# Kernel optimization log

Measured on AMD Instinct MI355X. Metric: run time of the kernel, lower is better.

## Reference

```python
import jax, jax.numpy as jnp
import numpy as np

B, S, F, D = 64, 129, 768, 4
MOM = 0.9
EPS = 1e-6


def setup_inputs() -> dict:
    key = jax.random.key(0)
    ks = jax.random.split(key, 8)
    x = jax.random.normal(ks[0], (B, S, F), dtype=jnp.float32)
    labels = jax.random.randint(ks[1], (B,), 0, 16, dtype=jnp.int32)
    domain = jax.random.randint(ks[2], (B,), 0, D, dtype=jnp.int32)
    lmda = jax.random.beta(ks[3], 0.1, 0.1, (B, 1, 1)).astype(jnp.float32)
    d_rand = jax.random.randint(ks[4], (B,), 1, D, dtype=jnp.int32)  # range(1, num_domains)
    mean_buf = (0.1 * jax.random.normal(ks[5], (D, F))).astype(jnp.float32)
    var_buf = jax.random.uniform(ks[6], (D, F), minval=0.5, maxval=1.5, dtype=jnp.float32)
    hg_noise = jax.random.normal(ks[7], (B, S, F), dtype=jnp.float32)
    return {"input": x, "lmda": lmda, "mean_buf": mean_buf, "var_buf": var_buf,
            "hg_noise": hg_noise, "labels": labels, "domain": domain, "d_rand": d_rand}


def reference(input, lmda, mean_buf, var_buf, hg_noise, labels, domain, d_rand):
    x = input  # [B,S,F]
    b, s, f = x.shape
    d = mean_buf.shape[0]

    # --- per-domain mean/var over dims [0,1] (unbiased), momentum buffer update ---
    tok = x.reshape(b * s, f)
    seg = jnp.repeat(domain, s)  # [B*S]
    cnt = jax.ops.segment_sum(jnp.ones((b * s,), x.dtype), seg, num_segments=d)  # tokens/domain
    s1 = jax.ops.segment_sum(tok, seg, num_segments=d)          # [D,F]
    s2 = jax.ops.segment_sum(tok * tok, seg, num_segments=d)    # [D,F]
    n = cnt[:, None]
    mu_d = s1 / jnp.maximum(n, 1.0)
    var_d = (s2 - n * mu_d * mu_d) / jnp.maximum(n - 1.0, 1.0)  # unbiased, matches torch.var
    present = (cnt > 0)[:, None]
    new_mean = jnp.where(present, MOM * mean_buf + (1.0 - MOM) * mu_d, mean_buf)
    new_var = jnp.where(present, MOM * var_buf + (1.0 - MOM) * var_d, var_buf)

    # --- instance renorm over token dim (unbiased var) + cross-domain restyle ---
    mu_i = x.mean(1, keepdims=True)
    v_i = x.var(1, keepdims=True, ddof=1)
    x_normed = (x - mu_i) * jax.lax.rsqrt(v_i + EPS)
    ds = (domain + d_rand) % d
    x_new = x_normed * jnp.sqrt(new_var[ds] + EPS)[:, None, :] + new_mean[ds][:, None, :]
    x_mix = lmda * x + (1.0 - lmda) * x_new

    # --- Gaussian hallucinated samples from own-domain stats ---
    hg = new_mean[domain][:, None, :] + jnp.sqrt(new_var[domain] + EPS)[:, None, :] * hg_noise

    # --- pairwise euclidean distance + hard example mining + soft-margin triplet loss ---
    xe = jnp.concatenate([x, x_mix, hg], axis=0).reshape(3 * b, s * f)  # [3B, S*F]
    ln = jnp.concatenate([labels, labels, -jnp.ones((b,), labels.dtype)])
    sq = jnp.sum(xe * xe, axis=1)
    d2 = sq[:, None] + sq[None, :] - 2.0 * (xe @ xe.T)
    dist = jnp.sqrt(jnp.clip(d2, 1e-12))
    pos = ln[:, None] == ln[None, :]
    big = jnp.asarray(1e30, dist.dtype)
    dist_ap = jnp.max(jnp.where(pos, dist, -big), axis=1)
    dist_an = jnp.min(jnp.where(pos, big, dist), axis=1)
    tri_hard_loss = jnp.mean(jax.nn.softplus(dist_ap - dist_an))  # SoftMarginLoss, y=1

    return x_mix, tri_hard_loss, new_mean, new_var
```

## Files before the change

### kernel.cpp

```cpp
#include <hip/hip_runtime.h>
#include <math.h>

#define B_ 64
#define S_ 129
#define F_ 768
#define N3 192
#define GSZ 36864
#define GRID_MAIN 252

#define WS_S1   0
#define WS_S2   49152
#define WS_PART 98304

#define OUT_LOSS 6340608
#define OUT_NM   6340609
#define OUT_NV   6343681

typedef unsigned int uint;
using short8v = __attribute__((ext_vector_type(8))) short;
using float4v = __attribute__((ext_vector_type(4))) float;

__global__ void k_stats(const float* __restrict__ x,
                        float* __restrict__ s1, float* __restrict__ s2,
                        float* __restrict__ out_loss) {
    __shared__ float4 r1[256], r2[256];
    if (blockIdx.x == 0 && threadIdx.x == 0) out_loss[0] = 0.0f;
    int b = blockIdx.x / 3, fg = blockIdx.x % 3;
    int c = threadIdx.x & 63, sp = threadIdx.x >> 6;
    int f = fg * 256 + c * 4;
    const float* p = x + (size_t)b * S_ * F_ + f;
    int s0 = sp * 32;
    int se = s0 + 32 + (sp == 3 ? 1 : 0);
    float4 a1 = {0.f,0.f,0.f,0.f}, a2 = {0.f,0.f,0.f,0.f};
#pragma unroll 4
    for (int s = s0; s < se; ++s) {
        float4 v = *(const float4*)(p + s * F_);
        a1.x += v.x; a1.y += v.y; a1.z += v.z; a1.w += v.w;
        a2.x += v.x*v.x; a2.y += v.y*v.y; a2.z += v.z*v.z; a2.w += v.w*v.w;
    }
    r1[threadIdx.x] = a1; r2[threadIdx.x] = a2;
    __syncthreads();
    if (sp == 0) {
        float4 t1 = r1[c], t2 = r2[c];
#pragma unroll
        for (int k = 1; k < 4; ++k) {
            float4 u1 = r1[k * 64 + c], u2 = r2[k * 64 + c];
            t1.x += u1.x; t1.y += u1.y; t1.z += u1.z; t1.w += u1.w;
            t2.x += u2.x; t2.y += u2.y; t2.z += u2.z; t2.w += u2.w;
        }
        *(float4*)(s1 + b * F_ + f) = t1;
        *(float4*)(s2 + b * F_ + f) = t2;
    }
}

__device__ __forceinline__ uint pack2(float a, float b) {
    uint ua = __float_as_uint(a);
    uint ub = __float_as_uint(b);
    uint ha = (ua + 0x7FFFu + ((ua >> 16) & 1u)) >> 16;
    uint hb = (ub + 0x7FFFu + ((ub >> 16) & 1u)) & 0xFFFF0000u;
    return hb | ha;
}

__device__ __forceinline__ void bf16_store8(char* lds, int row, int g,
                                            float4 v0, float4 v1) {
    uint4 H;
    H.x = pack2(v0.x, v0.y);
    H.y = pack2(v0.z, v0.w);
    H.z = pack2(v1.x, v1.y);
    H.w = pack2(v1.z, v1.w);
    *(uint4*)(lds + row * 128 + ((g ^ (row & 7)) << 4)) = H;
}

__device__ __forceinline__ float4 fma4(float4 a, float4 x, float4 b) {
    float4 r;
    r.x = fmaf(a.x, x.x, b.x); r.y = fmaf(a.y, x.y, b.y);
    r.z = fmaf(a.z, x.z, b.z); r.w = fmaf(a.w, x.w, b.w);
    return r;
}

template <bool EXCL>
__global__ __launch_bounds__(512, 2)
void k_main(const float* __restrict__ x, const float* __restrict__ hgn,
            const float* __restrict__ s1, const float* __restrict__ s2,
            const float* __restrict__ mean_buf, const float* __restrict__ var_buf,
            const float* __restrict__ lmda, const int* __restrict__ domain,
            const int* __restrict__ d_rand,
            float* __restrict__ xmix, float* __restrict__ out_nm,
            float* __restrict__ out_nv,
            float* part, int npart) {
    __shared__ __align__(16) char LDS[25088];
    __shared__ float NMV[4][64];
    __shared__ float SVV[4][64];

    int tid = threadIdx.x;
    int bid = blockIdx.x;
    int fc = bid % 12, sb = bid / 12;
    int f0 = fc * 64;
    int b = tid >> 3, g = tid & 7;
    int w = tid >> 6;
    int wr = (w >> 2) * 96, wc = (w & 3) * 48;
    int lane = tid & 63, m = lane & 15, qd = lane >> 4;

    int s = sb;
    size_t goff = ((size_t)b * S_ + s) * F_ + f0 + (g << 3);
    float4 X0 = ((const float4*)(x + goff))[0];
    float4 X1 = ((const float4*)(x + goff))[1];
    float4 N0 = ((const float4*)(hgn + goff))[0];
    float4 N1 = ((const float4*)(hgn + goff))[1];

    if (tid < 256) {
        int d = tid & 3, fl = tid >> 2;
        int f = f0 + fl;
        float a1 = 0.f, a2 = 0.f, cnt = 0.f;
#pragma unroll 8
        for (int bb = 0; bb < B_; ++bb) {
            bool mk = (domain[bb] == d);
            a1  += mk ? s1[bb * F_ + f] : 0.f;
            a2  += mk ? s2[bb * F_ + f] : 0.f;
            cnt += mk ? 1.f : 0.f;
        }
        float nm, nv;
        if (cnt > 0.f) {
            float n = cnt * (float)S_;
            float mu = a1 / n;
            float var = (a2 - n * mu * mu) / fmaxf(n - 1.f, 1.f);
            nm = 0.9f * mean_buf[d * F_ + f] + 0.1f * mu;
            nv = 0.9f * var_buf[d * F_ + f] + 0.1f * var;
        } else {
            nm = mean_buf[d * F_ + f];
            nv = var_buf[d * F_ + f];
        }
        NMV[d][fl] = nm;
        SVV[d][fl] = sqrtf(nv + 1e-6f);
        if (sb == 0) { out_nm[d * F_ + f] = nm; out_nv[d * F_ + f] = nv; }
    }
    __syncthreads();

    int cb = b * F_ + f0 + (g << 3);
    float4 S1a = ((const float4*)(s1 + cb))[0], S1b = ((const float4*)(s1 + cb))[1];
    float4 S2a = ((const float4*)(s2 + cb))[0], S2b = ((const float4*)(s2 + cb))[1];
    int dm = domain[b];
    int dsd = (dm + d_rand[b]) & 3;
    float lam = lmda[b];
    float4 C1a, C1b, C0a, C0b, HMa, HMb, HSa, HSb;
#define COEF(SC1, SC2, FL, RC1, RC0, RHM, RHS) {            \
        float mu = (SC1) * (1.0f / (float)S_);              \
        float v  = ((SC2) - (float)S_ * mu * mu) * (1.0f / (float)(S_ - 1)); \
        float r  = rsqrtf(v + 1e-6f);                       \
        float sv = SVV[dsd][FL];                            \
        float rs = r * sv;                                  \
        RC1 = lam + (1.0f - lam) * rs;                      \
        RC0 = (1.0f - lam) * (NMV[dsd][FL] - mu * rs);      \
        RHM = NMV[dm][FL];                                  \
        RHS = SVV[dm][FL]; }
    {
        int fb = g << 3;
        COEF(S1a.x, S2a.x, fb + 0, C1a.x, C0a.x, HMa.x, HSa.x);
        COEF(S1a.y, S2a.y, fb + 1, C1a.y, C0a.y, HMa.y, HSa.y);
        COEF(S1a.z, S2a.z, fb + 2, C1a.z, C0a.z, HMa.z, HSa.z);
        COEF(S1a.w, S2a.w, fb + 3, C1a.w, C0a.w, HMa.w, HSa.w);
        COEF(S1b.x, S2b.x, fb + 4, C1b.x, C0b.x, HMb.x, HSb.x);
        COEF(S1b.y, S2b.y, fb + 5, C1b.y, C0b.y, HMb.y, HSb.y);
        COEF(S1b.z, S2b.z, fb + 6, C1b.z, C0b.z, HMb.z, HSb.z);
        COEF(S1b.w, S2b.w, fb + 7, C1b.w, C0b.w, HMb.w, HSb.w);
    }
#undef COEF

    float4v acc[6][3];
#pragma unroll
    for (int i = 0; i < 6; ++i)
#pragma unroll
        for (int j = 0; j < 3; ++j)
            acc[i][j] = (float4v){0.f, 0.f, 0.f, 0.f};

    for (; s < S_; s += 21) {
        float4 M0 = fma4(C1a, X0, C0a);
        float4 M1 = fma4(C1b, X1, C0b);
        ((float4*)(xmix + goff))[0] = M0;
        ((float4*)(xmix + goff))[1] = M1;
        float4 H0 = fma4(HSa, N0, HMa);
        float4 H1 = fma4(HSb, N1, HMb);

        bf16_store8(LDS, b, g, X0, X1);
        bf16_store8(LDS, 64 + b, g, M0, M1);
        bf16_store8(LDS, 128 + b, g, H0, H1);
        __syncthreads();

        int sn = s + 21;
        if (sn < S_) {
            goff = ((size_t)b * S_ + sn) * F_ + f0 + (g << 3);
            X0 = ((const float4*)(x + goff))[0];
            X1 = ((const float4*)(x + goff))[1];
            N0 = ((const float4*)(hgn + goff))[0];
            N1 = ((const float4*)(hgn + goff))[1];
        }

#pragma unroll
        for (int t = 0; t < 2; ++t) {
            short8v A[6];
#pragma unroll
            for (int i = 0; i < 6; ++i) {
                int row = wr + i * 16 + m;
                int go = (((t << 2) + qd) ^ (row & 7)) << 4;
                A[i] = *(const short8v*)(LDS + row * 128 + go);
            }
#pragma unroll
            for (int j = 0; j < 3; ++j) {
                int row = wc + j * 16 + m;
                int go = (((t << 2) + qd) ^ (row & 7)) << 4;
                short8v Bv = *(const short8v*)(LDS + row * 128 + go);
#pragma unroll
                for (int i = 0; i < 6; ++i)
                    acc[i][j] = __builtin_amdgcn_mfma_f32_16x16x32_bf16(A[i], Bv, acc[i][j], 0, 0, 0);
            }
        }
        __syncthreads();
    }

    float* T = (float*)LDS;
    const int PADW = 196;
    float* dst = part + (size_t)(bid % npart) * GSZ;
    int lrb = (wr ? 16 : 0) + (qd << 2);
    int lr2 = tid >> 4;
#pragma unroll
    for (int i = 0; i < 6; ++i) {
        __syncthreads();
#pragma unroll
        for (int j = 0; j < 3; ++j) {
            int colb = wc + j * 16 + m;
#pragma unroll
            for (int r = 0; r < 4; ++r)
                T[(lrb + r) * PADW + colb] = acc[i][j][r];
        }
        __syncthreads();
        int grow = i * 16 + (lr2 & 15) + (lr2 >> 4) * 96;
#pragma unroll
        for (int k = 0; k < 3; ++k) {
            int c4 = k * 16 + (tid & 15);
            float4 vv = *(const float4*)&T[lr2 * PADW + (c4 << 2)];
            int o = grow * N3 + (c4 << 2);
            if (EXCL) {
                *(float4*)(dst + o) = vv;
            } else {
                atomicAdd(dst + o + 0, vv.x);
                atomicAdd(dst + o + 1, vv.y);
                atomicAdd(dst + o + 2, vv.z);
                atomicAdd(dst + o + 3, vv.w);
            }
        }
    }
}

__global__ void k_red(const float* __restrict__ part, float* __restrict__ gram, int npart) {
    int j = blockIdx.x * 256 + threadIdx.x;
    float s = 0.0f;
#pragma unroll 8
    for (int p = 0; p < npart; ++p) s += part[(size_t)p * GSZ + j];
    gram[j] = s;
}

__global__ void k_loss(const float* __restrict__ gram, const int* __restrict__ labels,
                       float* __restrict__ out_loss) {
    __shared__ float sq[N3];
    __shared__ int ln[N3];
    int i = blockIdx.x, lane = threadIdx.x;
    for (int k = lane; k < N3; k += 64) {
        sq[k] = gram[k * (N3 + 1)];
        ln[k] = (k < 128) ? labels[k & 63] : -1;
    }
    __syncthreads();
    int li = ln[i];
    float si = sq[i];
    float ap = -1e30f, an = 1e30f;
    for (int j = lane; j < N3; j += 64) {
        float d2 = si + sq[j] - 2.0f * gram[i * N3 + j];
        float dist = sqrtf(fmaxf(d2, 1e-12f));
        bool pos = (li == ln[j]);
        ap = pos ? fmaxf(ap, dist) : ap;
        an = pos ? an : fminf(an, dist);
    }
#pragma unroll
    for (int off = 32; off; off >>= 1) {
        ap = fmaxf(ap, __shfl_xor(ap, off));
        an = fminf(an, __shfl_xor(an, off));
    }
    if (lane == 0) {
        float xv = ap - an;
        float sp = fmaxf(xv, 0.0f) + log1pf(expf(-fabsf(xv)));
        atomicAdd(out_loss, sp * (1.0f / (float)N3));
    }
}

extern "C" void kernel_launch(void* const* d_in, const int* in_sizes, int n_in,
                              void* d_out, int out_size, void* d_ws, size_t ws_size,
                              hipStream_t stream) {
    const float* x        = (const float*)d_in[0];
    const float* lmda     = (const float*)d_in[1];
    const float* mean_buf = (const float*)d_in[2];
    const float* var_buf  = (const float*)d_in[3];
    const float* hgn      = (const float*)d_in[4];
    const int*   labels   = (const int*)d_in[5];
    const int*   domain   = (const int*)d_in[6];
    const int*   d_rand   = (const int*)d_in[7];
    float* out = (float*)d_out;
    float* ws  = (float*)d_ws;

    long avail = (long)(ws_size / 4) - WS_PART;
    int npart = (int)(avail / GSZ) - 1;
    if (npart < 1) npart = 1;
    if (npart > GRID_MAIN) npart = GRID_MAIN;
    bool excl = (npart == GRID_MAIN);
    float* part = ws + WS_PART;
    float* gram = ws + WS_PART + (size_t)npart * GSZ;

    k_stats<<<dim3(192), dim3(256), 0, stream>>>(x, ws + WS_S1, ws + WS_S2,
                                                 out + OUT_LOSS);
    if (!excl) {
        hipMemsetAsync(part, 0, (size_t)npart * GSZ * 4, stream);
    }
    if (excl) {
        k_main<true><<<dim3(GRID_MAIN), dim3(512), 0, stream>>>(
            x, hgn, ws + WS_S1, ws + WS_S2, mean_buf, var_buf,
            lmda, domain, d_rand,
            out, out + OUT_NM, out + OUT_NV, part, npart);
    } else {
        k_main<false><<<dim3(GRID_MAIN), dim3(512), 0, stream>>>(
            x, hgn, ws + WS_S1, ws + WS_S2, mean_buf, var_buf,
            lmda, domain, d_rand,
            out, out + OUT_NM, out + OUT_NV, part, npart);
    }
    k_red<<<dim3(144), dim3(256), 0, stream>>>(part, gram, npart);
    k_loss<<<dim3(N3), dim3(64), 0, stream>>>(gram, labels, out + OUT_LOSS);
}
```

Before: 154.2 us.

## Fuse stats, gram, reduction and loss into one cooperative kernel with grid syncs

Replaces the multi-kernel pipeline (stats kernel, main gram kernel, separate reduction and loss kernels) with a single cooperative launch that uses grid.sync between phases. The stats phase now spreads each block's token loop over 512 threads, and the partial-gram reduction plus triplet loss run inside the same kernel. The aim is to remove kernel launch gaps and inter-kernel idle time. The cost is grid-wide barriers, and it depends on cooperative launch succeeding with all 252 blocks resident, with the old path kept as a fallback.

Result: slower. 262.9 us (+70.5%).

```diff
diff --git a/kernel.cpp b/kernel.cpp
--- a/kernel.cpp
+++ b/kernel.cpp
@@ -1,5 +1,8 @@
 #include <hip/hip_runtime.h>
+#include <hip/hip_cooperative_groups.h>
 #include <math.h>
+
+namespace cg = cooperative_groups;
 
 #define B_ 64
 #define S_ 129
@@ -10,7 +13,8 @@
 
 #define WS_S1   0
 #define WS_S2   49152
-#define WS_PART 98304
+#define WS_SQ   98304
+#define WS_PART 98560
 
 #define OUT_LOSS 6340608
 #define OUT_NM   6340609
@@ -19,6 +23,285 @@
 typedef unsigned int uint;
 using short8v = __attribute__((ext_vector_type(8))) short;
 using float4v = __attribute__((ext_vector_type(4))) float;
+
+__device__ __forceinline__ uint pack2(float a, float b) {
+    uint ua = __float_as_uint(a);
+    uint ub = __float_as_uint(b);
+    uint ha = (ua + 0x7FFFu + ((ua >> 16) & 1u)) >> 16;
+    uint hb = (ub + 0x7FFFu + ((ub >> 16) & 1u)) & 0xFFFF0000u;
+    return hb | ha;
+}
+
+__device__ __forceinline__ void bf16_store8(char* lds, int row, int g,
+                                            float4 v0, float4 v1) {
+    uint4 H;
+    H.x = pack2(v0.x, v0.y);
+    H.y = pack2(v0.z, v0.w);
+    H.z = pack2(v1.x, v1.y);
+    H.w = pack2(v1.z, v1.w);
+    *(uint4*)(lds + row * 128 + ((g ^ (row & 7)) << 4)) = H;
+}
+
+__device__ __forceinline__ float4 fma4(float4 a, float4 x, float4 b) {
+    float4 r;
+    r.x = fmaf(a.x, x.x, b.x); r.y = fmaf(a.y, x.y, b.y);
+    r.z = fmaf(a.z, x.z, b.z); r.w = fmaf(a.w, x.w, b.w);
+    return r;
+}
+
+__global__ __launch_bounds__(512, 2)
+void k_all(const float* __restrict__ x, const float* __restrict__ hgn,
+           const float* __restrict__ mean_buf, const float* __restrict__ var_buf,
+           const float* __restrict__ lmda, const int* __restrict__ domain,
+           const int* __restrict__ d_rand, const int* __restrict__ labels,
+           float* __restrict__ xmix, float* __restrict__ out_nm,
+           float* __restrict__ out_nv, float* __restrict__ out_loss,
+           float* __restrict__ s1, float* __restrict__ s2,
+           float* __restrict__ sqw, float* part) {
+    __shared__ __align__(16) char LDS[32768];
+    __shared__ float NMV[4][64];
+    __shared__ float SVV[4][64];
+
+    cg::grid_group grid = cg::this_grid();
+    int tid = threadIdx.x;
+    int bid = blockIdx.x;
+
+    if (bid < 192) {
+        float4* r1 = (float4*)LDS;
+        float4* r2 = (float4*)(LDS + 8192);
+        int bb = bid / 3, fg = bid % 3;
+        int c = tid & 63, sp = tid >> 6;
+        int f = fg * 256 + c * 4;
+        const float* p = x + (size_t)bb * S_ * F_ + f;
+        int s0 = sp * 16;
+        int se = s0 + 16 + (sp == 7 ? 1 : 0);
+        float4 a1 = {0.f,0.f,0.f,0.f}, a2 = {0.f,0.f,0.f,0.f};
+#pragma unroll 4
+        for (int s = s0; s < se; ++s) {
+            float4 v = *(const float4*)(p + s * F_);
+            a1.x += v.x; a1.y += v.y; a1.z += v.z; a1.w += v.w;
+            a2.x += v.x*v.x; a2.y += v.y*v.y; a2.z += v.z*v.z; a2.w += v.w*v.w;
+        }
+        r1[tid] = a1; r2[tid] = a2;
+        __syncthreads();
+        if (sp == 0) {
+            float4 t1 = r1[c], t2 = r2[c];
+#pragma unroll
+            for (int k = 1; k < 8; ++k) {
+                float4 u1 = r1[k * 64 + c], u2 = r2[k * 64 + c];
+                t1.x += u1.x; t1.y += u1.y; t1.z += u1.z; t1.w += u1.w;
+                t2.x += u2.x; t2.y += u2.y; t2.z += u2.z; t2.w += u2.w;
+            }
+            *(float4*)(s1 + bb * F_ + f) = t1;
+            *(float4*)(s2 + bb * F_ + f) = t2;
+        }
+    }
+    grid.sync();
+
+    {
+        int fc = bid % 12, sb = bid / 12;
+        int f0 = fc * 64;
+        int b = tid >> 3, g = tid & 7;
+        int w = tid >> 6;
+        int wr = (w >> 2) * 96, wc = (w & 3) * 48;
+        int lane = tid & 63, m = lane & 15, qd = lane >> 4;
+
+        int s = sb;
+        size_t goff = ((size_t)b * S_ + s) * F_ + f0 + (g << 3);
+        float4 X0 = ((const float4*)(x + goff))[0];
+        float4 X1 = ((const float4*)(x + goff))[1];
+        float4 N0 = ((const float4*)(hgn + goff))[0];
+        float4 N1 = ((const float4*)(hgn + goff))[1];
+
+        if (tid < 256) {
+            int d = tid & 3, fl = tid >> 2;
+            int f = f0 + fl;
+            float a1 = 0.f, a2 = 0.f, cnt = 0.f;
+#pragma unroll 8
+            for (int bb = 0; bb < B_; ++bb) {
+                bool mk = (domain[bb] == d);
+                a1  += mk ? s1[bb * F_ + f] : 0.f;
+                a2  += mk ? s2[bb * F_ + f] : 0.f;
+                cnt += mk ? 1.f : 0.f;
+            }
+            float nm, nv;
+            if (cnt > 0.f) {
+                float n = cnt * (float)S_;
+                float mu = a1 / n;
+                float var = (a2 - n * mu * mu) / fmaxf(n - 1.f, 1.f);
+                nm = 0.9f * mean_buf[d * F_ + f] + 0.1f * mu;
+                nv = 0.9f * var_buf[d * F_ + f] + 0.1f * var;
+            } else {
+                nm = mean_buf[d * F_ + f];
+                nv = var_buf[d * F_ + f];
+            }
+            NMV[d][fl] = nm;
+            SVV[d][fl] = sqrtf(nv + 1e-6f);
+            if (sb == 0) { out_nm[d * F_ + f] = nm; out_nv[d * F_ + f] = nv; }
+        }
+        __syncthreads();
+
+        int cb = b * F_ + f0 + (g << 3);
+        float4 S1a = ((const float4*)(s1 + cb))[0], S1b = ((const float4*)(s1 + cb))[1];
+        float4 S2a = ((const float4*)(s2 + cb))[0], S2b = ((const float4*)(s2 + cb))[1];
+        int dm = domain[b];
+        int dsd = (dm + d_rand[b]) & 3;
+        float lam = lmda[b];
+        float4 C1a, C1b, C0a, C0b, HMa, HMb, HSa, HSb;
+#define COEF(SC1, SC2, FL, RC1, RC0, RHM, RHS) {            \
+        float mu = (SC1) * (1.0f / (float)S_);              \
+        float v  = ((SC2) - (float)S_ * mu * mu) * (1.0f / (float)(S_ - 1)); \
+        float r  = rsqrtf(v + 1e-6f);                       \
+        float sv = SVV[dsd][FL];                            \
+        float rs = r * sv;                                  \
+        RC1 = lam + (1.0f - lam) * rs;                      \
+        RC0 = (1.0f - lam) * (NMV[dsd][FL] - mu * rs);      \
+        RHM = NMV[dm][FL];                                  \
+        RHS = SVV[dm][FL]; }
+        {
+            int fb = g << 3;
+            COEF(S1a.x, S2a.x, fb + 0, C1a.x, C0a.x, HMa.x, HSa.x);
+            COEF(S1a.y, S2a.y, fb + 1, C1a.y, C0a.y, HMa.y, HSa.y);
+            COEF(S1a.z, S2a.z, fb + 2, C1a.z, C0a.z, HMa.z, HSa.z);
+            COEF(S1a.w, S2a.w, fb + 3, C1a.w, C0a.w, HMa.w, HSa.w);
+            COEF(S1b.x, S2b.x, fb + 4, C1b.x, C0b.x, HMb.x, HSb.x);
+            COEF(S1b.y, S2b.y, fb + 5, C1b.y, C0b.y, HMb.y, HSb.y);
+            COEF(S1b.z, S2b.z, fb + 6, C1b.z, C0b.z, HMb.z, HSb.z);
+            COEF(S1b.w, S2b.w, fb + 7, C1b.w, C0b.w, HMb.w, HSb.w);
+        }
+#undef COEF
+
+        float4v acc[6][3];
+#pragma unroll
+        for (int i = 0; i < 6; ++i)
+#pragma unroll
+            for (int j = 0; j < 3; ++j)
+                acc[i][j] = (float4v){0.f, 0.f, 0.f, 0.f};
+
+        for (; s < S_; s += 21) {
+            float4 M0 = fma4(C1a, X0, C0a);
+            float4 M1 = fma4(C1b, X1, C0b);
+            ((float4*)(xmix + goff))[0] = M0;
+            ((float4*)(xmix + goff))[1] = M1;
+            float4 H0 = fma4(HSa, N0, HMa);
+            float4 H1 = fma4(HSb, N1, HMb);
+
+            bf16_store8(LDS, b, g, X0, X1);
+            bf16_store8(LDS, 64 + b, g, M0, M1);
+            bf16_store8(LDS, 128 + b, g, H0, H1);
+            __syncthreads();
+
+            int sn = s + 21;
+            if (sn < S_) {
+                goff = ((size_t)b * S_ + sn) * F_ + f0 + (g << 3);
+                X0 = ((const float4*)(x + goff))[0];
+                X1 = ((const float4*)(x + goff))[1];
+                N0 = ((const float4*)(hgn + goff))[0];
+                N1 = ((const float4*)(hgn + goff))[1];
+            }
+
+#pragma unroll
+            for (int t = 0; t < 2; ++t) {
+                short8v A[6];
+#pragma unroll
+                for (int i = 0; i < 6; ++i) {
+                    int row = wr + i * 16 + m;
+                    int go = (((t << 2) + qd) ^ (row & 7)) << 4;
+                    A[i] = *(const short8v*)(LDS + row * 128 + go);
+                }
+#pragma unroll
+                for (int j = 0; j < 3; ++j) {
+                    int row = wc + j * 16 + m;
+                    int go = (((t << 2) + qd) ^ (row & 7)) << 4;
+                    short8v Bv = *(const short8v*)(LDS + row * 128 + go);
+#pragma unroll
+                    for (int i = 0; i < 6; ++i)
+                        acc[i][j] = __builtin_amdgcn_mfma_f32_16x16x32_bf16(A[i], Bv, acc[i][j], 0, 0, 0);
+                }
+            }
+            __syncthreads();
+        }
+
+        float* T = (float*)LDS;
+        const int PADW = 196;
+        float* dst = part + (size_t)bid * GSZ;
+        int lrb = (wr ? 16 : 0) + (qd << 2);
+        int lr2 = tid >> 4;
+#pragma unroll
+        for (int i = 0; i < 6; ++i) {
+            __syncthreads();
+#pragma unroll
+            for (int j = 0; j < 3; ++j) {
+                int colb = wc + j * 16 + m;
+#pragma unroll
+                for (int r = 0; r < 4; ++r)
+                    T[(lrb + r) * PADW + colb] = acc[i][j][r];
+            }
+            __syncthreads();
+            int grow = i * 16 + (lr2 & 15) + (lr2 >> 4) * 96;
+#pragma unroll
+            for (int k = 0; k < 3; ++k) {
+                int c4 = k * 16 + (tid & 15);
+                float4 vv = *(const float4*)&T[lr2 * PADW + (c4 << 2)];
+                *(float4*)(dst + grow * N3 + (c4 << 2)) = vv;
+            }
+        }
+    }
+    grid.sync();
+
+    float* ROW = (float*)LDS;
+    if (bid == 0 && tid == 0) out_loss[0] = 0.0f;
+    if (bid < N3 && tid < 384) {
+        int c = tid % 192, half = tid / 192;
+        float sacc = 0.f;
+#pragma unroll 8
+        for (int p = half; p < GRID_MAIN; p += 2)
+            sacc += part[(size_t)p * GSZ + bid * N3 + c];
+        ROW[half * 192 + c] = sacc;
+    }
+    __syncthreads();
+    if (bid < N3 && tid < 192) {
+        float rv = ROW[tid] + ROW[192 + tid];
+        ROW[tid] = rv;
+        if (tid == bid) sqw[bid] = rv;
+    }
+    grid.sync();
+
+    if (bid < N3) {
+        float* SQS = (float*)(LDS + 2048);
+        int*   LN  = (int*)(LDS + 2048 + 768);
+        float* APW = (float*)(LDS + 4096);
+        float* ANW = (float*)(LDS + 4096 + 16);
+        if (tid < N3) {
+            SQS[tid] = sqw[tid];
+            LN[tid] = (tid < 128) ? labels[tid & 63] : -1;
+        }
+        __syncthreads();
+        float ap = -1e30f, an = 1e30f;
+        if (tid < N3) {
+            int li = LN[bid];
+            float d2 = SQS[bid] + SQS[tid] - 2.0f * ROW[tid];
+            float dist = sqrtf(fmaxf(d2, 1e-12f));
+            bool pos = (li == LN[tid]);
+            ap = pos ? dist : -1e30f;
+            an = pos ? 1e30f : dist;
+        }
+#pragma unroll
+        for (int off = 32; off; off >>= 1) {
+            ap = fmaxf(ap, __shfl_xor(ap, off));
+            an = fminf(an, __shfl_xor(an, off));
+        }
+        if (tid < N3 && (tid & 63) == 0) { APW[tid >> 6] = ap; ANW[tid >> 6] = an; }
+        __syncthreads();
+        if (tid == 0) {
+            float a = fmaxf(fmaxf(APW[0], APW[1]), APW[2]);
+            float n = fminf(fminf(ANW[0], ANW[1]), ANW[2]);
+            float xv = a - n;
+            float sp = fmaxf(xv, 0.0f) + log1pf(expf(-fabsf(xv)));
+            atomicAdd(out_loss, sp * (1.0f / (float)N3));
+        }
+    }
+}
 
 __global__ void k_stats(const float* __restrict__ x,
                         float* __restrict__ s1, float* __restrict__ s2,
@@ -51,31 +334,6 @@
         *(float4*)(s1 + b * F_ + f) = t1;
         *(float4*)(s2 + b * F_ + f) = t2;
     }
-}
-
-__device__ __forceinline__ uint pack2(float a, float b) {
-    uint ua = __float_as_uint(a);
-    uint ub = __float_as_uint(b);
-    uint ha = (ua + 0x7FFFu + ((ua >> 16) & 1u)) >> 16;
-    uint hb = (ub + 0x7FFFu + ((ub >> 16) & 1u)) & 0xFFFF0000u;
-    return hb | ha;
-}
-
-__device__ __forceinline__ void bf16_store8(char* lds, int row, int g,
-                                            float4 v0, float4 v1) {
-    uint4 H;
-    H.x = pack2(v0.x, v0.y);
-    H.y = pack2(v0.z, v0.w);
-    H.z = pack2(v1.x, v1.y);
-    H.w = pack2(v1.z, v1.w);
-    *(uint4*)(lds + row * 128 + ((g ^ (row & 7)) << 4)) = H;
-}
-
-__device__ __forceinline__ float4 fma4(float4 a, float4 x, float4 b) {
-    float4 r;
-    r.x = fmaf(a.x, x.x, b.x); r.y = fmaf(a.y, x.y, b.y);
-    r.z = fmaf(a.z, x.z, b.z); r.w = fmaf(a.w, x.w, b.w);
-    return r;
 }
 
 template <bool EXCL>
@@ -305,7 +563,28 @@
     float* out = (float*)d_out;
     float* ws  = (float*)d_ws;
 
-    long avail = (long)(ws_size / 4) - WS_PART;
+    long ws_floats = (long)(ws_size / 4);
+    bool coop_ok = false;
+    if (ws_floats >= WS_PART + (long)GRID_MAIN * GSZ) {
+        float* xmix = out;
+        float* onm  = out + OUT_NM;
+        float* onv  = out + OUT_NV;
+        float* ols  = out + OUT_LOSS;
+        float* s1p  = ws + WS_S1;
+        float* s2p  = ws + WS_S2;
+        float* sqp  = ws + WS_SQ;
+        float* pp   = ws + WS_PART;
+        void* args[] = {(void*)&x, (void*)&hgn, (void*)&mean_buf, (void*)&var_buf,
+                        (void*)&lmda, (void*)&domain, (void*)&d_rand, (void*)&labels,
+                        (void*)&xmix, (void*)&onm, (void*)&onv, (void*)&ols,
+                        (void*)&s1p, (void*)&s2p, (void*)&sqp, (void*)&pp};
+        hipError_t e = hipLaunchCooperativeKernel((void*)k_all, dim3(GRID_MAIN),
+                                                  dim3(512), args, 0, stream);
+        coop_ok = (e == hipSuccess);
+    }
+    if (coop_ok) return;
+
+    long avail = ws_floats - WS_PART;
     int npart = (int)(avail / GSZ) - 1;
     if (npart < 1) npart = 1;
     if (npart > GRID_MAIN) npart = GRID_MAIN;
```

## Fuse gram reduction into loss kernel and double-buffer main-loop loads

Applied to the files above, without the earlier changes.

Removes the separate partial-gram reduction kernel. Each loss block now sums its own gram row across all partials, and the diagonal (squared norms) is gathered by atomics from the main kernel into a small workspace vector. The main kernel prefetches two token slices ahead with alternating register sets to deepen load latency hiding, and the stats kernel uses 512 threads with shorter per-thread loops. This trades one launch and the full gram round-trip for more register pressure in the main kernel and larger loss blocks that each read every partial row.

Result: faster. 141.9 us (-8.0%).

```diff
diff --git a/kernel.cpp b/kernel.cpp
--- a/kernel.cpp
+++ b/kernel.cpp
@@ -10,7 +10,8 @@
 
 #define WS_S1   0
 #define WS_S2   49152
-#define WS_PART 98304
+#define WS_SQ   98304
+#define WS_PART 98560
 
 #define OUT_LOSS 6340608
 #define OUT_NM   6340609
@@ -19,39 +20,6 @@
 typedef unsigned int uint;
 using short8v = __attribute__((ext_vector_type(8))) short;
 using float4v = __attribute__((ext_vector_type(4))) float;
-
-__global__ void k_stats(const float* __restrict__ x,
-                        float* __restrict__ s1, float* __restrict__ s2,
-                        float* __restrict__ out_loss) {
-    __shared__ float4 r1[256], r2[256];
-    if (blockIdx.x == 0 && threadIdx.x == 0) out_loss[0] = 0.0f;
-    int b = blockIdx.x / 3, fg = blockIdx.x % 3;
-    int c = threadIdx.x & 63, sp = threadIdx.x >> 6;
-    int f = fg * 256 + c * 4;
-    const float* p = x + (size_t)b * S_ * F_ + f;
-    int s0 = sp * 32;
-    int se = s0 + 32 + (sp == 3 ? 1 : 0);
-    float4 a1 = {0.f,0.f,0.f,0.f}, a2 = {0.f,0.f,0.f,0.f};
-#pragma unroll 4
-    for (int s = s0; s < se; ++s) {
-        float4 v = *(const float4*)(p + s * F_);
-        a1.x += v.x; a1.y += v.y; a1.z += v.z; a1.w += v.w;
-        a2.x += v.x*v.x; a2.y += v.y*v.y; a2.z += v.z*v.z; a2.w += v.w*v.w;
-    }
-    r1[threadIdx.x] = a1; r2[threadIdx.x] = a2;
-    __syncthreads();
-    if (sp == 0) {
-        float4 t1 = r1[c], t2 = r2[c];
-#pragma unroll
-        for (int k = 1; k < 4; ++k) {
-            float4 u1 = r1[k * 64 + c], u2 = r2[k * 64 + c];
-            t1.x += u1.x; t1.y += u1.y; t1.z += u1.z; t1.w += u1.w;
-            t2.x += u2.x; t2.y += u2.y; t2.z += u2.z; t2.w += u2.w;
-        }
-        *(float4*)(s1 + b * F_ + f) = t1;
-        *(float4*)(s2 + b * F_ + f) = t2;
-    }
-}
 
 __device__ __forceinline__ uint pack2(float a, float b) {
     uint ua = __float_as_uint(a);
@@ -76,6 +44,42 @@
     r.x = fmaf(a.x, x.x, b.x); r.y = fmaf(a.y, x.y, b.y);
     r.z = fmaf(a.z, x.z, b.z); r.w = fmaf(a.w, x.w, b.w);
     return r;
+}
+
+__global__ void k_stats(const float* __restrict__ x,
+                        float* __restrict__ s1, float* __restrict__ s2,
+                        float* __restrict__ sqw, float* __restrict__ out_loss) {
+    __shared__ float4 r1[512], r2[512];
+    if (blockIdx.x == 0) {
+        if (threadIdx.x == 0) out_loss[0] = 0.0f;
+        if (threadIdx.x < N3) sqw[threadIdx.x] = 0.0f;
+    }
+    int b = blockIdx.x / 3, fg = blockIdx.x % 3;
+    int c = threadIdx.x & 63, sp = threadIdx.x >> 6;
+    int f = fg * 256 + c * 4;
+    const float* p = x + (size_t)b * S_ * F_ + f;
+    int s0 = sp * 16;
+    int se = s0 + 16 + (sp == 7 ? 1 : 0);
+    float4 a1 = {0.f,0.f,0.f,0.f}, a2 = {0.f,0.f,0.f,0.f};
+#pragma unroll 4
+    for (int s = s0; s < se; ++s) {
+        float4 v = *(const float4*)(p + s * F_);
+        a1.x += v.x; a1.y += v.y; a1.z += v.z; a1.w += v.w;
+        a2.x += v.x*v.x; a2.y += v.y*v.y; a2.z += v.z*v.z; a2.w += v.w*v.w;
+    }
+    r1[threadIdx.x] = a1; r2[threadIdx.x] = a2;
+    __syncthreads();
+    if (sp == 0) {
+        float4 t1 = r1[c], t2 = r2[c];
+#pragma unroll
+        for (int k = 1; k < 8; ++k) {
+            float4 u1 = r1[k * 64 + c], u2 = r2[k * 64 + c];
+            t1.x += u1.x; t1.y += u1.y; t1.z += u1.z; t1.w += u1.w;
+            t2.x += u2.x; t2.y += u2.y; t2.z += u2.z; t2.w += u2.w;
+        }
+        *(float4*)(s1 + b * F_ + f) = t1;
+        *(float4*)(s2 + b * F_ + f) = t2;
+    }
 }
 
 template <bool EXCL>
@@ -87,7 +91,7 @@
             const int* __restrict__ d_rand,
             float* __restrict__ xmix, float* __restrict__ out_nm,
             float* __restrict__ out_nv,
-            float* part, int npart) {
+            float* part, float* __restrict__ sqw, int npart) {
     __shared__ __align__(16) char LDS[25088];
     __shared__ float NMV[4][64];
     __shared__ float SVV[4][64];
@@ -101,12 +105,16 @@
     int wr = (w >> 2) * 96, wc = (w & 3) * 48;
     int lane = tid & 63, m = lane & 15, qd = lane >> 4;
 
-    int s = sb;
-    size_t goff = ((size_t)b * S_ + s) * F_ + f0 + (g << 3);
-    float4 X0 = ((const float4*)(x + goff))[0];
-    float4 X1 = ((const float4*)(x + goff))[1];
-    float4 N0 = ((const float4*)(hgn + goff))[0];
-    float4 N1 = ((const float4*)(hgn + goff))[1];
+    size_t gA = ((size_t)b * S_ + sb) * F_ + f0 + (g << 3);
+    float4 XA0 = ((const float4*)(x + gA))[0];
+    float4 XA1 = ((const float4*)(x + gA))[1];
+    float4 NA0 = ((const float4*)(hgn + gA))[0];
+    float4 NA1 = ((const float4*)(hgn + gA))[1];
+    size_t gB = ((size_t)b * S_ + sb + 21) * F_ + f0 + (g << 3);
+    float4 XB0 = ((const float4*)(x + gB))[0];
+    float4 XB1 = ((const float4*)(x + gB))[1];
+    float4 NB0 = ((const float4*)(hgn + gB))[0];
+    float4 NB1 = ((const float4*)(hgn + gB))[1];
 
     if (tid < 256) {
         int d = tid & 3, fl = tid >> 2;
@@ -173,53 +181,63 @@
         for (int j = 0; j < 3; ++j)
             acc[i][j] = (float4v){0.f, 0.f, 0.f, 0.f};
 
-    for (; s < S_; s += 21) {
-        float4 M0 = fma4(C1a, X0, C0a);
-        float4 M1 = fma4(C1b, X1, C0b);
-        ((float4*)(xmix + goff))[0] = M0;
-        ((float4*)(xmix + goff))[1] = M1;
-        float4 H0 = fma4(HSa, N0, HMa);
-        float4 H1 = fma4(HSb, N1, HMb);
-
-        bf16_store8(LDS, b, g, X0, X1);
-        bf16_store8(LDS, 64 + b, g, M0, M1);
-        bf16_store8(LDS, 128 + b, g, H0, H1);
-        __syncthreads();
-
-        int sn = s + 21;
-        if (sn < S_) {
-            goff = ((size_t)b * S_ + sn) * F_ + f0 + (g << 3);
-            X0 = ((const float4*)(x + goff))[0];
-            X1 = ((const float4*)(x + goff))[1];
-            N0 = ((const float4*)(hgn + goff))[0];
-            N1 = ((const float4*)(hgn + goff))[1];
-        }
-
-#pragma unroll
-        for (int t = 0; t < 2; ++t) {
-            short8v A[6];
-#pragma unroll
-            for (int i = 0; i < 6; ++i) {
-                int row = wr + i * 16 + m;
-                int go = (((t << 2) + qd) ^ (row & 7)) << 4;
-                A[i] = *(const short8v*)(LDS + row * 128 + go);
-            }
-#pragma unroll
-            for (int j = 0; j < 3; ++j) {
-                int row = wc + j * 16 + m;
-                int go = (((t << 2) + qd) ^ (row & 7)) << 4;
-                short8v Bv = *(const short8v*)(LDS + row * 128 + go);
-#pragma unroll
-                for (int i = 0; i < 6; ++i)
-                    acc[i][j] = __builtin_amdgcn_mfma_f32_16x16x32_bf16(A[i], Bv, acc[i][j], 0, 0, 0);
-            }
-        }
-        __syncthreads();
-    }
+#define MFMA_SECTION                                                         \
+        _Pragma("unroll")                                                    \
+        for (int t = 0; t < 2; ++t) {                                        \
+            short8v A[6];                                                    \
+            _Pragma("unroll")                                                \
+            for (int i = 0; i < 6; ++i) {                                    \
+                int row = wr + i * 16 + m;                                   \
+                int go = (((t << 2) + qd) ^ (row & 7)) << 4;                 \
+                A[i] = *(const short8v*)(LDS + row * 128 + go);              \
+            }                                                                \
+            _Pragma("unroll")                                                \
+            for (int j = 0; j < 3; ++j) {                                    \
+                int row = wc + j * 16 + m;                                   \
+                int go = (((t << 2) + qd) ^ (row & 7)) << 4;                 \
+                short8v Bv = *(const short8v*)(LDS + row * 128 + go);        \
+                _Pragma("unroll")                                            \
+                for (int i = 0; i < 6; ++i)                                  \
+                    acc[i][j] = __builtin_amdgcn_mfma_f32_16x16x32_bf16(     \
+                        A[i], Bv, acc[i][j], 0, 0, 0);                       \
+            }                                                                \
+        }
+
+#define DO_CHUNK(X0_, X1_, N0_, N1_, GOFF_, SNXT_)                           \
+    {                                                                        \
+        float4 M0 = fma4(C1a, X0_, C0a);                                     \
+        float4 M1 = fma4(C1b, X1_, C0b);                                     \
+        ((float4*)(xmix + GOFF_))[0] = M0;                                   \
+        ((float4*)(xmix + GOFF_))[1] = M1;                                   \
+        float4 H0 = fma4(HSa, N0_, HMa);                                     \
+        float4 H1 = fma4(HSb, N1_, HMb);                                     \
+        bf16_store8(LDS, b, g, X0_, X1_);                                    \
+        bf16_store8(LDS, 64 + b, g, M0, M1);                                 \
+        bf16_store8(LDS, 128 + b, g, H0, H1);                                \
+        __syncthreads();                                                     \
+        if ((SNXT_) < S_) {                                                  \
+            GOFF_ = ((size_t)b * S_ + (SNXT_)) * F_ + f0 + (g << 3);         \
+            X0_ = ((const float4*)(x + GOFF_))[0];                           \
+            X1_ = ((const float4*)(x + GOFF_))[1];                           \
+            N0_ = ((const float4*)(hgn + GOFF_))[0];                         \
+            N1_ = ((const float4*)(hgn + GOFF_))[1];                         \
+        }                                                                    \
+        MFMA_SECTION                                                         \
+        __syncthreads();                                                     \
+    }
+
+    for (int s = sb; s < S_; s += 42) {
+        DO_CHUNK(XA0, XA1, NA0, NA1, gA, s + 42);
+        if (s + 21 < S_) {
+            DO_CHUNK(XB0, XB1, NB0, NB1, gB, s + 63);
+        }
+    }
+#undef DO_CHUNK
+#undef MFMA_SECTION
 
     float* T = (float*)LDS;
     const int PADW = 196;
-    float* dst = part + (size_t)(bid % npart) * GSZ;
+    float* dst = part + (size_t)(EXCL ? bid : (bid % npart)) * GSZ;
     int lrb = (wr ? 16 : 0) + (qd << 2);
     int lr2 = tid >> 4;
 #pragma unroll
@@ -248,44 +266,55 @@
                 atomicAdd(dst + o + 3, vv.w);
             }
         }
-    }
-}
-
-__global__ void k_red(const float* __restrict__ part, float* __restrict__ gram, int npart) {
-    int j = blockIdx.x * 256 + threadIdx.x;
-    float s = 0.0f;
-#pragma unroll 8
-    for (int p = 0; p < npart; ++p) s += part[(size_t)p * GSZ + j];
-    gram[j] = s;
-}
-
-__global__ void k_loss(const float* __restrict__ gram, const int* __restrict__ labels,
-                       float* __restrict__ out_loss) {
-    __shared__ float sq[N3];
-    __shared__ int ln[N3];
-    int i = blockIdx.x, lane = threadIdx.x;
-    for (int k = lane; k < N3; k += 64) {
-        sq[k] = gram[k * (N3 + 1)];
-        ln[k] = (k < 128) ? labels[k & 63] : -1;
+        if (tid < 32) {
+            int dr = i * 16 + (tid & 15) + (tid >> 4) * 96;
+            atomicAdd(sqw + dr, T[tid * PADW + dr]);
+        }
+    }
+}
+
+__global__ void k_loss(const float* __restrict__ part, const float* __restrict__ sqw,
+                       const int* __restrict__ labels,
+                       float* __restrict__ out_loss, int npart) {
+    __shared__ float ROW[2][N3];
+    __shared__ float SQS[N3];
+    __shared__ int   LN[N3];
+    __shared__ float APW[3], ANW[3];
+    int i = blockIdx.x, tid = threadIdx.x;
+    if (tid < 384) {
+        int c = tid % N3, h = tid / N3;
+        float sacc = 0.f;
+#pragma unroll 4
+        for (int p = h; p < npart; p += 2)
+            sacc += part[(size_t)p * GSZ + i * N3 + c];
+        ROW[h][c] = sacc;
+    }
+    if (tid >= 320) {
+        int c = tid - 320;
+        SQS[c] = sqw[c];
+        LN[c] = (c < 128) ? labels[c & 63] : -1;
     }
     __syncthreads();
-    int li = ln[i];
-    float si = sq[i];
-    float ap = -1e30f, an = 1e30f;
-    for (int j = lane; j < N3; j += 64) {
-        float d2 = si + sq[j] - 2.0f * gram[i * N3 + j];
+    if (tid < N3) {
+        float gij = ROW[0][tid] + ROW[1][tid];
+        int li = LN[i];
+        float d2 = SQS[i] + SQS[tid] - 2.0f * gij;
         float dist = sqrtf(fmaxf(d2, 1e-12f));
-        bool pos = (li == ln[j]);
-        ap = pos ? fmaxf(ap, dist) : ap;
-        an = pos ? an : fminf(an, dist);
-    }
-#pragma unroll
-    for (int off = 32; off; off >>= 1) {
-        ap = fmaxf(ap, __shfl_xor(ap, off));
-        an = fminf(an, __shfl_xor(an, off));
-    }
-    if (lane == 0) {
-        float xv = ap - an;
+        bool pos = (li == LN[tid]);
+        float ap = pos ? dist : -1e30f;
+        float an = pos ? 1e30f : dist;
+#pragma unroll
+        for (int off = 32; off; off >>= 1) {
+            ap = fmaxf(ap, __shfl_xor(ap, off));
+            an = fminf(an, __shfl_xor(an, off));
+        }
+        if ((tid & 63) == 0) { APW[tid >> 6] = ap; ANW[tid >> 6] = an; }
+    }
+    __syncthreads();
+    if (tid == 0) {
+        float a = fmaxf(fmaxf(APW[0], APW[1]), APW[2]);
+        float n = fminf(fminf(ANW[0], ANW[1]), ANW[2]);
+        float xv = a - n;
         float sp = fmaxf(xv, 0.0f) + log1pf(expf(-fabsf(xv)));
         atomicAdd(out_loss, sp * (1.0f / (float)N3));
     }
@@ -306,15 +335,15 @@
     float* ws  = (float*)d_ws;
 
     long avail = (long)(ws_size / 4) - WS_PART;
-    int npart = (int)(avail / GSZ) - 1;
+    int npart = (int)(avail / GSZ);
     if (npart < 1) npart = 1;
     if (npart > GRID_MAIN) npart = GRID_MAIN;
     bool excl = (npart == GRID_MAIN);
     float* part = ws + WS_PART;
-    float* gram = ws + WS_PART + (size_t)npart * GSZ;
-
-    k_stats<<<dim3(192), dim3(256), 0, stream>>>(x, ws + WS_S1, ws + WS_S2,
-                                                 out + OUT_LOSS);
+    float* sqw  = ws + WS_SQ;
+
+    k_stats<<<dim3(192), dim3(512), 0, stream>>>(x, ws + WS_S1, ws + WS_S2,
+                                                 sqw, out + OUT_LOSS);
     if (!excl) {
         hipMemsetAsync(part, 0, (size_t)npart * GSZ * 4, stream);
     }
@@ -322,13 +351,13 @@
         k_main<true><<<dim3(GRID_MAIN), dim3(512), 0, stream>>>(
             x, hgn, ws + WS_S1, ws + WS_S2, mean_buf, var_buf,
             lmda, domain, d_rand,
-            out, out + OUT_NM, out + OUT_NV, part, npart);
+            out, out + OUT_NM, out + OUT_NV, part, sqw, npart);
     } else {
         k_main<false><<<dim3(GRID_MAIN), dim3(512), 0, stream>>>(
             x, hgn, ws + WS_S1, ws + WS_S2, mean_buf, var_buf,
             lmda, domain, d_rand,
-            out, out + OUT_NM, out + OUT_NV, part, npart);
-    }
-    k_red<<<dim3(144), dim3(256), 0, stream>>>(part, gram, npart);
-    k_loss<<<dim3(N3), dim3(64), 0, stream>>>(gram, labels, out + OUT_LOSS);
-}
+            out, out + OUT_NM, out + OUT_NV, part, sqw, npart);
+    }
+    k_loss<<<dim3(N3), dim3(512), 0, stream>>>(part, sqw, labels,
+                                               out + OUT_LOSS, npart);
+}
```
